# Performance work log

Measured on AMD Instinct MI355X. Metric: run time of the kernel, lower is better.

Reference implementation:

```python
import jax, jax.numpy as jnp
import numpy as np

B, N, D, H, DK, DV, R = 4, 256, 256, 8, 32, 32, 64
EPS = 1e-6


def setup_inputs() -> dict:
    key = jax.random.key(0)
    ks = jax.random.split(key, 16)
    s = D ** -0.5
    return {
        "q": jax.random.normal(ks[0], (B, N, D), jnp.float32),
        "k": jax.random.normal(ks[1], (B, N, D), jnp.float32),
        "v": jax.random.normal(ks[2], (B, N, D), jnp.float32),
        "mask": jax.random.randint(ks[3], (B, N, N), 0, 2).astype(jnp.int32),
        "link": jax.random.uniform(ks[4], (B, N, N, R), jnp.float32),
        "Wq": jax.random.normal(ks[5], (D, H * DK), jnp.float32) * s,
        "Wk": jax.random.normal(ks[6], (D, H * DK), jnp.float32) * s,
        "Wr": jax.random.normal(ks[7], (D, H * DK), jnp.float32) * s,
        "Wv": jax.random.normal(ks[8], (D, H * DV), jnp.float32) * s,
        "Wvv": jax.random.normal(ks[9], (D, H * DV), jnp.float32) * s,
        "relationE": jax.random.normal(ks[10], (R, D), jnp.float32) * s,
        "Wo": jax.random.normal(ks[11], (H * DV, D), jnp.float32) * s,
        "gamma": jnp.ones((D,), jnp.float32),
        "beta": jnp.zeros((D,), jnp.float32),
    }


def reference(q, k, v, mask, link, Wq, Wk, Wr, Wv, Wvv, relationE, Wo, gamma, beta):
    # rela_num != 0 branch of Ruleformer MultiHeadAttention (dropout = identity, eval mode).
    residual = q
    b, n, d = q.shape
    # per-head projections of X (== q == residual in this branch): [b,h,n,dk]
    Xq = (q @ Wq).reshape(b, n, H, DK).transpose(0, 2, 1, 3)
    Xk = (q @ Wk).reshape(b, n, H, DK).transpose(0, 2, 1, 3)
    Xv = (q @ Wv).reshape(b, n, H, DV).transpose(0, 2, 1, 3)

    # calcE: relation-biased scores. Rk[b,i,j,h,d] = (link @ relationE @ Wr)
    Rk = jnp.einsum('bijr,re->bije', link, relationE @ Wr).reshape(b, n, n, H, DK)
    # attn[b,h,i,j] = Xq[b,h,i] . (Xk[b,h,j] + Rk[b,i,j,h])
    attn = jnp.einsum('bhid,bhjd->bhij', Xq, Xk)
    attn = attn + jnp.einsum('bijhd,bhid->bhij', Rk, Xq)
    attn = attn / (DK ** 0.5)
    attn = jnp.where(mask[:, None, :, :] == 0, -1e9, attn)
    alpha = jax.nn.softmax(attn, axis=-1)  # [b,h,n,n]

    # calcZ: Z[b,h,i] = sum_j alpha[b,h,i,j] * (Xv[b,h,j] + Rv[b,i,j,h])
    Rv = jnp.einsum('bijr,re->bije', link, relationE @ Wvv).reshape(b, n, n, H, DV)
    Z = jnp.einsum('bhij,bhjd->bhid', alpha, Xv)
    Z = Z + jnp.einsum('bhij,bijhd->bhid', alpha, Rv)

    out = Z.transpose(0, 2, 1, 3).reshape(b, n, H * DV) @ Wo
    out = out + residual
    mu = out.mean(-1, keepdims=True)
    var = ((out - mu) ** 2).mean(-1, keepdims=True)
    out = (out - mu) * jax.lax.rsqrt(var + EPS) * gamma + beta
    return out, alpha
```

## Files before the change

kernel.cpp:

```cpp
#include <hip/hip_runtime.h>
#include <math.h>

constexpr int B_ = 4, N_ = 256, D_ = 256, H_ = 8, DK_ = 32, DV_ = 32, R_ = 64;
constexpr float SCALE_ = 0.17677669529663687f;
constexpr float EPS_ = 1e-6f;

__global__ __launch_bounds__(256) void ekev_kernel(
        const float* __restrict__ relE, const float* __restrict__ Wr,
        const float* __restrict__ Wvv, float* __restrict__ Ek,
        float* __restrict__ Ev) {
    int r = blockIdx.x & 63;
    int which = blockIdx.x >> 6;
    const float* W = which ? Wvv : Wr;
    float* out = which ? Ev : Ek;
    __shared__ float row[256];
    int tid = threadIdx.x;
    row[tid] = relE[r * 256 + tid];
    __syncthreads();
    float acc = 0.f;
    for (int d = 0; d < 256; ++d) acc += row[d] * W[d * 256 + tid];
    out[r * 256 + tid] = acc;
}

__global__ __launch_bounds__(256) void mcat_kernel(
        const float* __restrict__ Wq, const float* __restrict__ Ek,
        float* __restrict__ M) {
    int d = blockIdx.x;
    int t = threadIdx.x;
    __shared__ float wrow[256];
    wrow[t] = Wq[d * 256 + t];
    __syncthreads();
    for (int hr = t; hr < 512; hr += 256) {
        int h = hr >> 6, r = hr & 63;
        const float4* ek4 = (const float4*)(Ek + r * 256 + h * 32);
        const float4* w4 = (const float4*)(wrow + h * 32);
        float acc = 0.f;
#pragma unroll
        for (int k = 0; k < 8; ++k) {
            float4 e = ek4[k], w = w4[k];
            acc += e.x * w.x + e.y * w.y + e.z * w.z + e.w * w.w;
        }
        M[d * 512 + hr] = acc;
    }
}

__global__ __launch_bounds__(256) void projT_kernel(
        const float* __restrict__ q, const float* __restrict__ Wq,
        const float* __restrict__ Wk, const float* __restrict__ Wv,
        const float* __restrict__ M, float* __restrict__ Xq,
        float* __restrict__ Xk, float* __restrict__ Xv,
        float* __restrict__ T) {
    int ct = blockIdx.x >> 4, rt = blockIdx.x & 15;
    int t = threadIdx.x;
    __shared__ float ash[32 * 65];
    __shared__ float bsh[32 * 64];
    const float* W;
    int ncols, cbase;
    if (ct < 4)       { W = Wq; cbase = ct * 64;        ncols = 256; }
    else if (ct < 8)  { W = Wk; cbase = (ct - 4) * 64;  ncols = 256; }
    else if (ct < 12) { W = Wv; cbase = (ct - 8) * 64;  ncols = 256; }
    else              { W = M;  cbase = (ct - 12) * 64; ncols = 512; }
    int ti = t >> 4, tj = t & 15;
    float acc[4][4] = {{0.f}};
    for (int kc = 0; kc < 8; ++kc) {
        __syncthreads();
#pragma unroll
        for (int kk = 0; kk < 2; ++kk) {
            int m = t + kk * 256;
            int i = m >> 3, kq = m & 7;
            float4 v = *(const float4*)(q + (size_t)(rt * 64 + i) * 256 + kc * 32 + kq * 4);
            ash[(kq * 4 + 0) * 65 + i] = v.x;
            ash[(kq * 4 + 1) * 65 + i] = v.y;
            ash[(kq * 4 + 2) * 65 + i] = v.z;
            ash[(kq * 4 + 3) * 65 + i] = v.w;
        }
#pragma unroll
        for (int kk = 0; kk < 2; ++kk) {
            int m = t + kk * 256;
            int k = m >> 4, j4 = m & 15;
            float4 v = *(const float4*)(W + (size_t)(kc * 32 + k) * ncols + cbase + j4 * 4);
            *(float4*)(bsh + k * 64 + j4 * 4) = v;
        }
        __syncthreads();
#pragma unroll 8
        for (int k = 0; k < 32; ++k) {
            float4 av = *(const float4*)(ash + k * 65 + ti * 4);
            float4 bv = *(const float4*)(bsh + k * 64 + tj * 4);
            acc[0][0] += av.x * bv.x; acc[0][1] += av.x * bv.y;
            acc[0][2] += av.x * bv.z; acc[0][3] += av.x * bv.w;
            acc[1][0] += av.y * bv.x; acc[1][1] += av.y * bv.y;
            acc[1][2] += av.y * bv.z; acc[1][3] += av.y * bv.w;
            acc[2][0] += av.z * bv.x; acc[2][1] += av.z * bv.y;
            acc[2][2] += av.z * bv.z; acc[2][3] += av.z * bv.w;
            acc[3][0] += av.w * bv.x; acc[3][1] += av.w * bv.y;
            acc[3][2] += av.w * bv.z; acc[3][3] += av.w * bv.w;
        }
    }
    if (ct < 12) {
        float* dst = (ct < 4) ? Xq : (ct < 8) ? Xk : Xv;
        int gcol = (ct & 3) * 64 + tj * 4;
        int h = gcol >> 5, dk = gcol & 31;
#pragma unroll
        for (int a = 0; a < 4; ++a) {
            int row = rt * 64 + ti * 4 + a;
            int bb = row >> 8, n = row & 255;
            *(float4*)(dst + ((size_t)(bb * 8 + h) * 256 + n) * 32 + dk) =
                make_float4(acc[a][0], acc[a][1], acc[a][2], acc[a][3]);
        }
    } else {
        int gcol = (ct - 12) * 64 + tj * 4;
#pragma unroll
        for (int a = 0; a < 4; ++a) {
            int row = rt * 64 + ti * 4 + a;
            *(float4*)(T + (size_t)row * 512 + gcol) =
                make_float4(acc[a][0], acc[a][1], acc[a][2], acc[a][3]);
        }
    }
}

__global__ __launch_bounds__(256) void qk_kernel(
        const float* __restrict__ Xq, const float* __restrict__ Xk,
        float* __restrict__ qk) {
    int x = blockIdx.x;
    int jt = x & 3, it = (x >> 2) & 3, bh = x >> 4;
    int t = threadIdx.x;
    __shared__ float xqsh[32 * 64];
    __shared__ float xksh[32 * 64];
#pragma unroll
    for (int k = 0; k < 2; ++k) {
        int m = t + k * 256;
        int i = m >> 3, dq4 = m & 7;
        float4 v = *(const float4*)(Xq + ((size_t)(bh * 256 + it * 64 + i)) * 32 + dq4 * 4);
        xqsh[(dq4 * 4 + 0) * 64 + i] = v.x;
        xqsh[(dq4 * 4 + 1) * 64 + i] = v.y;
        xqsh[(dq4 * 4 + 2) * 64 + i] = v.z;
        xqsh[(dq4 * 4 + 3) * 64 + i] = v.w;
        float4 u = *(const float4*)(Xk + ((size_t)(bh * 256 + jt * 64 + i)) * 32 + dq4 * 4);
        xksh[(dq4 * 4 + 0) * 64 + i] = u.x;
        xksh[(dq4 * 4 + 1) * 64 + i] = u.y;
        xksh[(dq4 * 4 + 2) * 64 + i] = u.z;
        xksh[(dq4 * 4 + 3) * 64 + i] = u.w;
    }
    __syncthreads();
    int ti = t >> 4, tj = t & 15;
    float acc[4][4] = {{0.f}};
#pragma unroll 8
    for (int dk = 0; dk < 32; ++dk) {
        float4 av = *(const float4*)(xqsh + dk * 64 + ti * 4);
        float4 bv = *(const float4*)(xksh + dk * 64 + tj * 4);
        acc[0][0] += av.x * bv.x; acc[0][1] += av.x * bv.y;
        acc[0][2] += av.x * bv.z; acc[0][3] += av.x * bv.w;
        acc[1][0] += av.y * bv.x; acc[1][1] += av.y * bv.y;
        acc[1][2] += av.y * bv.z; acc[1][3] += av.y * bv.w;
        acc[2][0] += av.z * bv.x; acc[2][1] += av.z * bv.y;
        acc[2][2] += av.z * bv.z; acc[2][3] += av.z * bv.w;
        acc[3][0] += av.w * bv.x; acc[3][1] += av.w * bv.y;
        acc[3][2] += av.w * bv.z; acc[3][3] += av.w * bv.w;
    }
#pragma unroll
    for (int a = 0; a < 4; ++a) {
        int i = it * 64 + ti * 4 + a;
        *(float4*)(qk + ((size_t)(bh * 256 + i)) * 256 + jt * 64 + tj * 4) =
            make_float4(acc[a][0], acc[a][1], acc[a][2], acc[a][3]);
    }
}

__global__ __launch_bounds__(256) void bias_kernel(
        const float* __restrict__ link, const float* __restrict__ T,
        float* __restrict__ biasOut) {
    int x = blockIdx.x;
    int jt = x & 3, bi = x >> 2;
    int b = bi >> 8, i = bi & 255;
    int t = threadIdx.x;
    __shared__ float linksh[64 * 67];
    __shared__ float Tsh[512];
    __shared__ float part[4 * 512];
    Tsh[t] = T[(size_t)bi * 512 + t];
    Tsh[256 + t] = T[(size_t)bi * 512 + 256 + t];
    {
        const float4* lp = (const float4*)(link + ((size_t)(bi * 256 + jt * 64)) * 64);
#pragma unroll
        for (int k = 0; k < 4; ++k) {
            int m = t + k * 256;
            float4 v = lp[m];
            int j = m >> 4, c = (m & 15) * 4;
            float* dst = linksh + j * 67 + c;
            dst[0] = v.x; dst[1] = v.y; dst[2] = v.z; dst[3] = v.w;
        }
    }
    __syncthreads();
    int j = t & 63, rg = t >> 6;
    float pacc[8] = {0.f, 0.f, 0.f, 0.f, 0.f, 0.f, 0.f, 0.f};
    for (int rr = 0; rr < 16; ++rr) {
        int r = rg * 16 + rr;
        float lv = linksh[j * 67 + r];
#pragma unroll
        for (int h = 0; h < 8; ++h) pacc[h] += lv * Tsh[h * 64 + r];
    }
#pragma unroll
    for (int h = 0; h < 8; ++h) part[rg * 512 + h * 64 + j] = pacc[h];
    __syncthreads();
    int hp = t >> 6;
#pragma unroll
    for (int e = 0; e < 2; ++e) {
        int h = hp * 2 + e;
        float sum = part[h * 64 + j] + part[512 + h * 64 + j] +
                    part[1024 + h * 64 + j] + part[1536 + h * 64 + j];
        biasOut[((size_t)(b * 8 + h) * 256 + i) * 256 + jt * 64 + j] = sum;
    }
}

__global__ __launch_bounds__(256) void smsp_kernel(
        const float* __restrict__ qk, const int* __restrict__ mask,
        const float* __restrict__ link, float* __restrict__ alpha,
        float* __restrict__ S) {
    int bi = blockIdx.x;
    int b = bi >> 8, i = bi & 255;
    int t = threadIdx.x;
    __shared__ float ashm[2048];
    __shared__ float part[2048];
    __shared__ float redsh[64];

    int j = t;
    float s[8];
#pragma unroll
    for (int h = 0; h < 8; ++h) {
        size_t off = ((size_t)(b * 8 + h) * 256 + i) * 256 + j;
        s[h] = (qk[off] + alpha[off]) * SCALE_;
    }
    if (mask[(b * 256 + i) * 256 + j] == 0) {
#pragma unroll
        for (int h = 0; h < 8; ++h) s[h] = -1e9f;
    }
    int lane = t & 63, wv = t >> 6;
#pragma unroll
    for (int h = 0; h < 8; ++h) {
        float v = s[h];
        for (int off = 32; off > 0; off >>= 1) v = fmaxf(v, __shfl_xor(v, off));
        if (lane == 0) redsh[h * 4 + wv] = v;
    }
    __syncthreads();
    float mx[8];
#pragma unroll
    for (int h = 0; h < 8; ++h)
        mx[h] = fmaxf(fmaxf(redsh[h * 4 + 0], redsh[h * 4 + 1]),
                      fmaxf(redsh[h * 4 + 2], redsh[h * 4 + 3]));
    __syncthreads();
#pragma unroll
    for (int h = 0; h < 8; ++h) {
        float e = __expf(s[h] - mx[h]);
        s[h] = e;
        float v = e;
        for (int off = 32; off > 0; off >>= 1) v += __shfl_xor(v, off);
        if (lane == 0) redsh[32 + h * 4 + wv] = v;
    }
    __syncthreads();
#pragma unroll
    for (int h = 0; h < 8; ++h) {
        float esum = redsh[32 + h * 4 + 0] + redsh[32 + h * 4 + 1] +
                     redsh[32 + h * 4 + 2] + redsh[32 + h * 4 + 3];
        float a = s[h] * (1.f / esum);
        ashm[h * 256 + j] = a;
        alpha[((size_t)(b * 8 + h) * 256 + i) * 256 + j] = a;
    }
    __syncthreads();

    int r = t & 63, g = t >> 6;
    float pacc[8] = {0.f, 0.f, 0.f, 0.f, 0.f, 0.f, 0.f, 0.f};
    const float* lp = link + ((size_t)(bi * 256 + g * 64)) * 64 + r;
#pragma unroll 4
    for (int j4 = 0; j4 < 16; ++j4) {
        float l0 = lp[(j4 * 4 + 0) * 64];
        float l1 = lp[(j4 * 4 + 1) * 64];
        float l2 = lp[(j4 * 4 + 2) * 64];
        float l3 = lp[(j4 * 4 + 3) * 64];
#pragma unroll
        for (int h = 0; h < 8; ++h) {
            float4 a = *(const float4*)(ashm + h * 256 + g * 64 + j4 * 4);
            pacc[h] += a.x * l0 + a.y * l1 + a.z * l2 + a.w * l3;
        }
    }
#pragma unroll
    for (int h = 0; h < 8; ++h) part[g * 512 + h * 64 + r] = pacc[h];
    __syncthreads();
    for (int hr = t; hr < 512; hr += 256) {
        S[(size_t)bi * 512 + hr] =
            part[hr] + part[512 + hr] + part[1024 + hr] + part[1536 + hr];
    }
}

__global__ __launch_bounds__(256) void zx_kernel(
        const float* __restrict__ alpha, const float* __restrict__ Xv,
        float* __restrict__ Zx) {
    int x = blockIdx.x;
    int it = x & 7, bh = x >> 3;
    int t = threadIdx.x;
    __shared__ float ashm[32 * 64];
    __shared__ float xvsh[64 * 32];
    int dv = t & 31, ig = t >> 5;
    float acc[4] = {0.f, 0.f, 0.f, 0.f};
    for (int cc = 0; cc < 4; ++cc) {
        __syncthreads();
#pragma unroll
        for (int k = 0; k < 2; ++k) {
            int m = t + k * 256;
            int i = m >> 4, jq = m & 15;
            float4 v = *(const float4*)(alpha + ((size_t)(bh * 256 + it * 32 + i)) * 256 + cc * 64 + jq * 4);
            float* dst = ashm + i * 64 + jq * 4;
            dst[0] = v.x; dst[1] = v.y; dst[2] = v.z; dst[3] = v.w;
            ((float4*)xvsh)[m] = *(const float4*)(Xv + ((size_t)(bh * 256 + cc * 64)) * 32 + m * 4);
        }
        __syncthreads();
        for (int j = 0; j < 64; ++j) {
            float xv = xvsh[j * 32 + dv];
#pragma unroll
            for (int ii = 0; ii < 4; ++ii)
                acc[ii] += ashm[(ig * 4 + ii) * 64 + j] * xv;
        }
    }
#pragma unroll
    for (int ii = 0; ii < 4; ++ii)
        Zx[((size_t)(bh * 256 + it * 32 + ig * 4 + ii)) * 32 + dv] = acc[ii];
}

__global__ __launch_bounds__(256) void outz_kernel(
        const float* __restrict__ S, const float* __restrict__ Zx,
        const float* __restrict__ Ev, const float* __restrict__ Wo,
        const float* __restrict__ q, const float* __restrict__ gamma,
        const float* __restrict__ beta, float* __restrict__ out) {
    int blk = blockIdx.x;
    int t = threadIdx.x;
    __shared__ float Ssh[4 * 512];
    __shared__ float zsh[4 * 256];
    __shared__ float redsh[32];
    for (int m = t; m < 2048; m += 256) {
        int rr = m >> 9, hr = m & 511;
        Ssh[m] = S[(size_t)(blk * 4 + rr) * 512 + hr];
    }
    __syncthreads();
    int h = t >> 5, dv = t & 31;
    int row0 = blk * 4;
    int b = row0 >> 8;
    float z[4];
#pragma unroll
    for (int rr = 0; rr < 4; ++rr) {
        int i = (row0 + rr) & 255;
        z[rr] = Zx[((size_t)((b * 8 + h) * 256 + i)) * 32 + dv];
    }
    for (int r = 0; r < 64; ++r) {
        float ev = Ev[r * 256 + h * 32 + dv];
#pragma unroll
        for (int rr = 0; rr < 4; ++rr) z[rr] += Ssh[rr * 512 + h * 64 + r] * ev;
    }
#pragma unroll
    for (int rr = 0; rr < 4; ++rr) zsh[rr * 256 + t] = z[rr];
    __syncthreads();
    float acc[4];
#pragma unroll
    for (int rr = 0; rr < 4; ++rr) acc[rr] = q[(row0 + rr) * 256 + t];
    for (int d4 = 0; d4 < 64; ++d4) {
        float w0 = Wo[(d4 * 4 + 0) * 256 + t];
        float w1 = Wo[(d4 * 4 + 1) * 256 + t];
        float w2 = Wo[(d4 * 4 + 2) * 256 + t];
        float w3 = Wo[(d4 * 4 + 3) * 256 + t];
#pragma unroll
        for (int rr = 0; rr < 4; ++rr) {
            float4 zv = *(const float4*)(zsh + rr * 256 + d4 * 4);
            acc[rr] += zv.x * w0 + zv.y * w1 + zv.z * w2 + zv.w * w3;
        }
    }
    int lane = t & 63, wv = t >> 6;
#pragma unroll
    for (int rr = 0; rr < 4; ++rr) {
        float v = acc[rr], v2 = acc[rr] * acc[rr];
        for (int off = 32; off > 0; off >>= 1) {
            v += __shfl_xor(v, off);
            v2 += __shfl_xor(v2, off);
        }
        if (lane == 0) {
            redsh[rr * 8 + wv] = v;
            redsh[rr * 8 + 4 + wv] = v2;
        }
    }
    __syncthreads();
#pragma unroll
    for (int rr = 0; rr < 4; ++rr) {
        float sum = redsh[rr * 8 + 0] + redsh[rr * 8 + 1] + redsh[rr * 8 + 2] + redsh[rr * 8 + 3];
        float sum2 = redsh[rr * 8 + 4] + redsh[rr * 8 + 5] + redsh[rr * 8 + 6] + redsh[rr * 8 + 7];
        float mu = sum * (1.f / 256.f);
        float var = sum2 * (1.f / 256.f) - mu * mu;
        float dev = acc[rr] - mu;
        out[(row0 + rr) * 256 + t] = dev * rsqrtf(var + EPS_) * gamma[t] + beta[t];
    }
}

extern "C" void kernel_launch(void* const* d_in, const int* in_sizes, int n_in,
                              void* d_out, int out_size, void* d_ws, size_t ws_size,
                              hipStream_t stream) {
    const float* q     = (const float*)d_in[0];
    const int*   mask  = (const int*)d_in[3];
    const float* link  = (const float*)d_in[4];
    const float* Wq    = (const float*)d_in[5];
    const float* Wk    = (const float*)d_in[6];
    const float* Wr    = (const float*)d_in[7];
    const float* Wv    = (const float*)d_in[8];
    const float* Wvv   = (const float*)d_in[9];
    const float* relE  = (const float*)d_in[10];
    const float* Wo    = (const float*)d_in[11];
    const float* gamma = (const float*)d_in[12];
    const float* beta  = (const float*)d_in[13];

    float* out   = (float*)d_out;
    float* alpha = out + B_ * N_ * D_;

    float* ws    = (float*)d_ws;
    float* Ek    = ws;
    float* Ev    = Ek + 16384;
    float* Mcat  = Ev + 16384;
    float* Xq    = Mcat + 131072;
    float* Xk    = Xq + 262144;
    float* Xv    = Xk + 262144;
    float* T     = Xv + 262144;
    float* qkbuf = T + 524288;
    float* S     = qkbuf + 2097152;
    float* Zx    = S + 524288;

    ekev_kernel<<<128, 256, 0, stream>>>(relE, Wr, Wvv, Ek, Ev);
    mcat_kernel<<<256, 256, 0, stream>>>(Wq, Ek, Mcat);
    projT_kernel<<<320, 256, 0, stream>>>(q, Wq, Wk, Wv, Mcat, Xq, Xk, Xv, T);
    qk_kernel<<<512, 256, 0, stream>>>(Xq, Xk, qkbuf);
    bias_kernel<<<4096, 256, 0, stream>>>(link, T, alpha);
    smsp_kernel<<<1024, 256, 0, stream>>>(qkbuf, mask, link, alpha, S);
    zx_kernel<<<256, 256, 0, stream>>>(alpha, Xv, Zx);
    outz_kernel<<<256, 256, 0, stream>>>(S, Zx, Ev, Wo, q, gamma, beta, out);
}
```

Before: 208.9 us.

## Fuse bias into softmax kernel and merge Z computation with output projection

Folds the relation-bias computation into the softmax/S kernel so the bias is built in shared memory rather than written to and reread from the alpha buffer. It also merges the alpha·Xv kernel with the output-projection/layernorm kernel, which removes the Zx intermediate and a launch. In exchange, the fused softmax kernel runs serially over four link chunks with more barriers and 4096 fewer blocks of parallelism. The new Z path reads Xv straight from global memory per row pair instead of tiling it.

```diff
diff --git a/kernel.cpp b/kernel.cpp
--- a/kernel.cpp
+++ b/kernel.cpp
@@ -165,68 +165,60 @@
     }
 }
 
-__global__ __launch_bounds__(256) void bias_kernel(
-        const float* __restrict__ link, const float* __restrict__ T,
-        float* __restrict__ biasOut) {
-    int x = blockIdx.x;
-    int jt = x & 3, bi = x >> 2;
+__global__ __launch_bounds__(256) void biassm_kernel(
+        const float* __restrict__ link, const float* __restrict__ Tg,
+        const float* __restrict__ qk, const int* __restrict__ mask,
+        float* __restrict__ alpha, float* __restrict__ S) {
+    int bi = blockIdx.x;
     int b = bi >> 8, i = bi & 255;
     int t = threadIdx.x;
     __shared__ float linksh[64 * 67];
     __shared__ float Tsh[512];
-    __shared__ float part[4 * 512];
-    Tsh[t] = T[(size_t)bi * 512 + t];
-    Tsh[256 + t] = T[(size_t)bi * 512 + 256 + t];
-    {
-        const float4* lp = (const float4*)(link + ((size_t)(bi * 256 + jt * 64)) * 64);
+    __shared__ float ashm[2048];
+    __shared__ float part[2048];
+    __shared__ float redsh[64];
+    Tsh[t] = Tg[(size_t)bi * 512 + t];
+    Tsh[256 + t] = Tg[(size_t)bi * 512 + 256 + t];
+
+    for (int c = 0; c < 4; ++c) {
+        __syncthreads();
+        const float4* lp = (const float4*)(link + ((size_t)(bi * 256 + c * 64)) * 64);
 #pragma unroll
         for (int k = 0; k < 4; ++k) {
             int m = t + k * 256;
             float4 v = lp[m];
-            int j = m >> 4, c = (m & 15) * 4;
-            float* dst = linksh + j * 67 + c;
+            int j = m >> 4, col = (m & 15) * 4;
+            float* dst = linksh + j * 67 + col;
             dst[0] = v.x; dst[1] = v.y; dst[2] = v.z; dst[3] = v.w;
         }
-    }
-    __syncthreads();
-    int j = t & 63, rg = t >> 6;
-    float pacc[8] = {0.f, 0.f, 0.f, 0.f, 0.f, 0.f, 0.f, 0.f};
-    for (int rr = 0; rr < 16; ++rr) {
-        int r = rg * 16 + rr;
-        float lv = linksh[j * 67 + r];
-#pragma unroll
-        for (int h = 0; h < 8; ++h) pacc[h] += lv * Tsh[h * 64 + r];
-    }
-#pragma unroll
-    for (int h = 0; h < 8; ++h) part[rg * 512 + h * 64 + j] = pacc[h];
-    __syncthreads();
-    int hp = t >> 6;
-#pragma unroll
-    for (int e = 0; e < 2; ++e) {
-        int h = hp * 2 + e;
-        float sum = part[h * 64 + j] + part[512 + h * 64 + j] +
-                    part[1024 + h * 64 + j] + part[1536 + h * 64 + j];
-        biasOut[((size_t)(b * 8 + h) * 256 + i) * 256 + jt * 64 + j] = sum;
-    }
-}
-
-__global__ __launch_bounds__(256) void smsp_kernel(
-        const float* __restrict__ qk, const int* __restrict__ mask,
-        const float* __restrict__ link, float* __restrict__ alpha,
-        float* __restrict__ S) {
-    int bi = blockIdx.x;
-    int b = bi >> 8, i = bi & 255;
-    int t = threadIdx.x;
-    __shared__ float ashm[2048];
-    __shared__ float part[2048];
-    __shared__ float redsh[64];
+        __syncthreads();
+        int j = t & 63, rg = t >> 6;
+        float pacc[8] = {0.f, 0.f, 0.f, 0.f, 0.f, 0.f, 0.f, 0.f};
+        for (int rr = 0; rr < 16; ++rr) {
+            int r = rg * 16 + rr;
+            float lv = linksh[j * 67 + r];
+#pragma unroll
+            for (int h = 0; h < 8; ++h) pacc[h] += lv * Tsh[h * 64 + r];
+        }
+#pragma unroll
+        for (int h = 0; h < 8; ++h) part[rg * 512 + h * 64 + j] = pacc[h];
+        __syncthreads();
+        if ((t >> 6) == c) {
+            int jj = t & 63;
+#pragma unroll
+            for (int h = 0; h < 8; ++h)
+                ashm[h * 256 + t] = part[h * 64 + jj] + part[512 + h * 64 + jj] +
+                                    part[1024 + h * 64 + jj] + part[1536 + h * 64 + jj];
+        }
+    }
+    __syncthreads();
 
     int j = t;
     float s[8];
 #pragma unroll
     for (int h = 0; h < 8; ++h) {
         size_t off = ((size_t)(b * 8 + h) * 256 + i) * 256 + j;
-        s[h] = (qk[off] + alpha[off]) * SCALE_;
+        s[h] = (qk[off] + ashm[h * 256 + j]) * SCALE_;
     }
     if (mask[(b * 256 + i) * 256 + j] == 0) {
 #pragma unroll
@@ -266,22 +258,22 @@
     __syncthreads();
 
     int r = t & 63, g = t >> 6;
-    float pacc[8] = {0.f, 0.f, 0.f, 0.f, 0.f, 0.f, 0.f, 0.f};
-    const float* lp = link + ((size_t)(bi * 256 + g * 64)) * 64 + r;
+    float pacc2[8] = {0.f, 0.f, 0.f, 0.f, 0.f, 0.f, 0.f, 0.f};
+    const float* lp2 = link + ((size_t)(bi * 256 + g * 64)) * 64 + r;
 #pragma unroll 4
     for (int j4 = 0; j4 < 16; ++j4) {
-        float l0 = lp[(j4 * 4 + 0) * 64];
-        float l1 = lp[(j4 * 4 + 1) * 64];
-        float l2 = lp[(j4 * 4 + 2) * 64];
-        float l3 = lp[(j4 * 4 + 3) * 64];
+        float l0 = lp2[(j4 * 4 + 0) * 64];
+        float l1 = lp2[(j4 * 4 + 1) * 64];
+        float l2 = lp2[(j4 * 4 + 2) * 64];
+        float l3 = lp2[(j4 * 4 + 3) * 64];
 #pragma unroll
         for (int h = 0; h < 8; ++h) {
             float4 a = *(const float4*)(ashm + h * 256 + g * 64 + j4 * 4);
-            pacc[h] += a.x * l0 + a.y * l1 + a.z * l2 + a.w * l3;
-        }
-    }
-#pragma unroll
-    for (int h = 0; h < 8; ++h) part[g * 512 + h * 64 + r] = pacc[h];
+            pacc2[h] += a.x * l0 + a.y * l1 + a.z * l2 + a.w * l3;
+        }
+    }
+#pragma unroll
+    for (int h = 0; h < 8; ++h) part[g * 512 + h * 64 + r] = pacc2[h];
     __syncthreads();
     for (int hr = t; hr < 512; hr += 256) {
         S[(size_t)bi * 512 + hr] =
@@ -289,90 +281,64 @@
     }
 }
 
-__global__ __launch_bounds__(256) void zx_kernel(
+__global__ __launch_bounds__(256) void zout_kernel(
         const float* __restrict__ alpha, const float* __restrict__ Xv,
-        float* __restrict__ Zx) {
-    int x = blockIdx.x;
-    int it = x & 7, bh = x >> 3;
-    int t = threadIdx.x;
-    __shared__ float ashm[32 * 64];
-    __shared__ float xvsh[64 * 32];
-    int dv = t & 31, ig = t >> 5;
-    float acc[4] = {0.f, 0.f, 0.f, 0.f};
-    for (int cc = 0; cc < 4; ++cc) {
-        __syncthreads();
-#pragma unroll
-        for (int k = 0; k < 2; ++k) {
-            int m = t + k * 256;
-            int i = m >> 4, jq = m & 15;
-            float4 v = *(const float4*)(alpha + ((size_t)(bh * 256 + it * 32 + i)) * 256 + cc * 64 + jq * 4);
-            float* dst = ashm + i * 64 + jq * 4;
-            dst[0] = v.x; dst[1] = v.y; dst[2] = v.z; dst[3] = v.w;
-            ((float4*)xvsh)[m] = *(const float4*)(Xv + ((size_t)(bh * 256 + cc * 64)) * 32 + m * 4);
-        }
-        __syncthreads();
-        for (int j = 0; j < 64; ++j) {
-            float xv = xvsh[j * 32 + dv];
-#pragma unroll
-            for (int ii = 0; ii < 4; ++ii)
-                acc[ii] += ashm[(ig * 4 + ii) * 64 + j] * xv;
-        }
-    }
-#pragma unroll
-    for (int ii = 0; ii < 4; ++ii)
-        Zx[((size_t)(bh * 256 + it * 32 + ig * 4 + ii)) * 32 + dv] = acc[ii];
-}
-
-__global__ __launch_bounds__(256) void outz_kernel(
-        const float* __restrict__ S, const float* __restrict__ Zx,
-        const float* __restrict__ Ev, const float* __restrict__ Wo,
-        const float* __restrict__ q, const float* __restrict__ gamma,
-        const float* __restrict__ beta, float* __restrict__ out) {
+        const float* __restrict__ S, const float* __restrict__ Ev,
+        const float* __restrict__ Wo, const float* __restrict__ q,
+        const float* __restrict__ gamma, const float* __restrict__ beta,
+        float* __restrict__ out) {
     int blk = blockIdx.x;
-    int t = threadIdx.x;
-    __shared__ float Ssh[4 * 512];
-    __shared__ float zsh[4 * 256];
-    __shared__ float redsh[32];
-    for (int m = t; m < 2048; m += 256) {
-        int rr = m >> 9, hr = m & 511;
-        Ssh[m] = S[(size_t)(blk * 4 + rr) * 512 + hr];
-    }
-    __syncthreads();
-    int h = t >> 5, dv = t & 31;
-    int row0 = blk * 4;
+    int row0 = blk * 2;
     int b = row0 >> 8;
-    float z[4];
-#pragma unroll
-    for (int rr = 0; rr < 4; ++rr) {
-        int i = (row0 + rr) & 255;
-        z[rr] = Zx[((size_t)((b * 8 + h) * 256 + i)) * 32 + dv];
-    }
-    for (int r = 0; r < 64; ++r) {
-        float ev = Ev[r * 256 + h * 32 + dv];
-#pragma unroll
-        for (int rr = 0; rr < 4; ++rr) z[rr] += Ssh[rr * 512 + h * 64 + r] * ev;
-    }
-#pragma unroll
-    for (int rr = 0; rr < 4; ++rr) zsh[rr * 256 + t] = z[rr];
-    __syncthreads();
-    float acc[4];
-#pragma unroll
-    for (int rr = 0; rr < 4; ++rr) acc[rr] = q[(row0 + rr) * 256 + t];
+    int t = threadIdx.x;
+    __shared__ float Ssh[2 * 512];
+    __shared__ float ashm[2 * 2048];
+    __shared__ float zsh[2 * 256];
+    __shared__ float redsh[16];
+    for (int m = t; m < 1024; m += 256)
+        Ssh[m] = S[(size_t)(row0 + (m >> 9)) * 512 + (m & 511)];
+    for (int m = t; m < 4096; m += 256) {
+        int rr = m >> 11, h = (m >> 8) & 7, j = m & 255;
+        ashm[m] = alpha[((size_t)(b * 8 + h) * 256 + ((row0 + rr) & 255)) * 256 + j];
+    }
+    __syncthreads();
+    {
+        int h = t >> 5, dv = t & 31;
+        float z0 = 0.f, z1 = 0.f;
+        const float* xv = Xv + ((size_t)(b * 8 + h) * 256) * 32 + dv;
+#pragma unroll 4
+        for (int j = 0; j < 256; ++j) {
+            float x = xv[j * 32];
+            z0 += ashm[h * 256 + j] * x;
+            z1 += ashm[2048 + h * 256 + j] * x;
+        }
+#pragma unroll 4
+        for (int r = 0; r < 64; ++r) {
+            float ev = Ev[r * 256 + h * 32 + dv];
+            z0 += Ssh[h * 64 + r] * ev;
+            z1 += Ssh[512 + h * 64 + r] * ev;
+        }
+        zsh[t] = z0;
+        zsh[256 + t] = z1;
+    }
+    __syncthreads();
+    float a0 = q[(size_t)row0 * 256 + t];
+    float a1 = q[(size_t)(row0 + 1) * 256 + t];
     for (int d4 = 0; d4 < 64; ++d4) {
         float w0 = Wo[(d4 * 4 + 0) * 256 + t];
         float w1 = Wo[(d4 * 4 + 1) * 256 + t];
         float w2 = Wo[(d4 * 4 + 2) * 256 + t];
         float w3 = Wo[(d4 * 4 + 3) * 256 + t];
-#pragma unroll
-        for (int rr = 0; rr < 4; ++rr) {
-            float4 zv = *(const float4*)(zsh + rr * 256 + d4 * 4);
-            acc[rr] += zv.x * w0 + zv.y * w1 + zv.z * w2 + zv.w * w3;
-        }
+        float4 z0v = *(const float4*)(zsh + d4 * 4);
+        float4 z1v = *(const float4*)(zsh + 256 + d4 * 4);
+        a0 += z0v.x * w0 + z0v.y * w1 + z0v.z * w2 + z0v.w * w3;
+        a1 += z1v.x * w0 + z1v.y * w1 + z1v.z * w2 + z1v.w * w3;
     }
     int lane = t & 63, wv = t >> 6;
-#pragma unroll
-    for (int rr = 0; rr < 4; ++rr) {
-        float v = acc[rr], v2 = acc[rr] * acc[rr];
+    float acc2[2] = {a0, a1};
+#pragma unroll
+    for (int rr = 0; rr < 2; ++rr) {
+        float v = acc2[rr], v2 = acc2[rr] * acc2[rr];
         for (int off = 32; off > 0; off >>= 1) {
             v += __shfl_xor(v, off);
             v2 += __shfl_xor(v2, off);
@@ -384,13 +350,13 @@
     }
     __syncthreads();
 #pragma unroll
-    for (int rr = 0; rr < 4; ++rr) {
+    for (int rr = 0; rr < 2; ++rr) {
         float sum = redsh[rr * 8 + 0] + redsh[rr * 8 + 1] + redsh[rr * 8 + 2] + redsh[rr * 8 + 3];
         float sum2 = redsh[rr * 8 + 4] + redsh[rr * 8 + 5] + redsh[rr * 8 + 6] + redsh[rr * 8 + 7];
         float mu = sum * (1.f / 256.f);
         float var = sum2 * (1.f / 256.f) - mu * mu;
-        float dev = acc[rr] - mu;
-        out[(row0 + rr) * 256 + t] = dev * rsqrtf(var + EPS_) * gamma[t] + beta[t];
+        float dev = acc2[rr] - mu;
+        out[(size_t)(row0 + rr) * 256 + t] = dev * rsqrtf(var + EPS_) * gamma[t] + beta[t];
     }
 }
 
@@ -423,14 +389,11 @@
     float* T     = Xv + 262144;
     float* qkbuf = T + 524288;
     float* S     = qkbuf + 2097152;
-    float* Zx    = S + 524288;
 
     ekev_kernel<<<128, 256, 0, stream>>>(relE, Wr, Wvv, Ek, Ev);
     mcat_kernel<<<256, 256, 0, stream>>>(Wq, Ek, Mcat);
     projT_kernel<<<320, 256, 0, stream>>>(q, Wq, Wk, Wv, Mcat, Xq, Xk, Xv, T);
     qk_kernel<<<512, 256, 0, stream>>>(Xq, Xk, qkbuf);
-    bias_kernel<<<4096, 256, 0, stream>>>(link, T, alpha);
-    smsp_kernel<<<1024, 256, 0, stream>>>(qkbuf, mask, link, alpha, S);
-    zx_kernel<<<256, 256, 0, stream>>>(alpha, Xv, Zx);
-    outz_kernel<<<256, 256, 0, stream>>>(S, Zx, Ev, Wo, q, gamma, beta, out);
-}
+    biassm_kernel<<<1024, 256, 0, stream>>>(link, T, qkbuf, mask, alpha, S);
+    zout_kernel<<<512, 256, 0, stream>>>(alpha, Xv, S, Ev, Wo, q, gamma, beta, out);
+}
```

After: 208.0 us. Within noise of the previous version (-0.4%).
